# Kernel tuning notes

Hardware: AMD Instinct MI355X
Metric: run time of the kernel (lower is better)

Reference implementation:

```python
import jax, jax.numpy as jnp
import numpy as np

D_MODEL, D_QKV, N_HEADS = 1024, 64, 16


def setup_inputs() -> dict:
    key = jax.random.key(0)
    k_x, k_qkv, k_out = jax.random.split(key, 3)
    X = jax.random.normal(k_x, (2, 2048, D_MODEL), dtype=jnp.float32)
    # nn.Linear(d_model, 3*d_qkv*n_heads, bias=False): store as (in, out) for X @ W
    W_qkv = jax.random.normal(k_qkv, (D_MODEL, 3 * D_QKV * N_HEADS), dtype=jnp.float32) * (D_MODEL ** -0.5)
    W_out = jax.random.normal(k_out, (D_QKV * N_HEADS, D_MODEL), dtype=jnp.float32) * ((D_QKV * N_HEADS) ** -0.5)
    return {"X": X, "W_qkv": W_qkv, "W_out": W_out}


def reference(X, W_qkv, W_out):
    b, s, _ = X.shape
    h, d = N_HEADS, D_QKV
    scale = d ** 0.5
    qkv = X @ W_qkv                          # [b, s, 3*h*d]
    # Faithful to torch: view(b, s, h, d, 3).unbind(-1) -> interleaved q/k/v layout
    qkv = qkv.reshape(b, s, h, d, 3)
    q, k, v = qkv[..., 0], qkv[..., 1], qkv[..., 2]   # each [b, s, h, d]
    scores = jnp.einsum("bqhd,bkhd->bhqk", q, k) / scale
    weights = jax.nn.softmax(scores, axis=-1)          # [b, h, s, s]
    attn = jnp.einsum("bhqk,bkhd->bqhd", weights, v)   # [b, s, h, d]
    return attn.reshape(b, s, h * d) @ W_out           # [b, s, d_model]
```

## Files before the change

kernel.cpp:

```cpp
#include <hip/hip_runtime.h>
#include <hip/hip_bf16.h>
#include <math.h>

typedef __bf16 bf16;
typedef __bf16 bf16x4 __attribute__((ext_vector_type(4)));
typedef __bf16 bf16x8 __attribute__((ext_vector_type(8)));
typedef float f32x4 __attribute__((ext_vector_type(4)));

#define MFMA16(a, b, c) __builtin_amdgcn_mfma_f32_16x16x32_bf16(a, b, c, 0, 0, 0)

constexpr int D_MODEL = 1024;
constexpr int N_QKV   = 3072;
constexpr int BATCH   = 2;
constexpr int SEQ     = 2048;
constexpr int NH      = 16;
constexpr int DH      = 64;
constexpr int M_TOT   = BATCH * SEQ;

__device__ __forceinline__ void gl_lds16(const bf16* g, bf16* l) {
    __builtin_amdgcn_global_load_lds(
        (const __attribute__((address_space(1))) void*)g,
        (__attribute__((address_space(3))) void*)l, 16, 0, 0);
}

__device__ __forceinline__ void transpose_tile(
    const float* __restrict__ in, bf16* __restrict__ out,
    int K, int N, int n0, int k0, bf16 (*T)[72], bool permute)
{
    const int tid = threadIdx.x;
    const int r   = tid >> 2;
    const int c4  = (tid & 3) * 16;

    const float* src = in + (size_t)(k0 + r) * N + n0 + c4;
    f32x4 v0 = *(const f32x4*)(src + 0);
    f32x4 v1 = *(const f32x4*)(src + 4);
    f32x4 v2 = *(const f32x4*)(src + 8);
    f32x4 v3 = *(const f32x4*)(src + 12);
    #pragma unroll
    for (int j = 0; j < 4; j++) {
        T[c4 + j][r]      = (bf16)v0[j];
        T[c4 + 4 + j][r]  = (bf16)v1[j];
        T[c4 + 8 + j][r]  = (bf16)v2[j];
        T[c4 + 12 + j][r] = (bf16)v3[j];
    }
    __syncthreads();
    int rowg = n0 + r;
    if (permute) {
        const int which = rowg % 3;
        const int h     = rowg / 192;
        const int d     = (rowg % 192) / 3;
        rowg = which * 1024 + h * 64 + d;
    }
    bf16* dst = out + (size_t)rowg * K + k0 + c4;
    *(bf16x8*)(dst)     = *(const bf16x8*)&T[r][c4];
    *(bf16x8*)(dst + 8) = *(const bf16x8*)&T[r][c4 + 8];
}

__global__ __launch_bounds__(256) void prepass_kernel(
    const float* __restrict__ X, const float* __restrict__ Wqkv,
    const float* __restrict__ Wout,
    bf16* __restrict__ xb, bf16* __restrict__ wqkv_t, bf16* __restrict__ wout_t)
{
    __shared__ bf16 T[64][72];
    const int b = blockIdx.x;
    if (b < 2048) {
        const size_t i = ((size_t)b * 256 + threadIdx.x) * 8;
        f32x4 a0 = *(const f32x4*)(X + i);
        f32x4 a1 = *(const f32x4*)(X + i + 4);
        bf16x8 w;
        #pragma unroll
        for (int j = 0; j < 4; j++) { w[j] = (bf16)a0[j]; w[j + 4] = (bf16)a1[j]; }
        *(bf16x8*)(xb + i) = w;
    } else if (b < 2048 + 768) {
        const int idx = b - 2048;
        transpose_tile(Wqkv, wqkv_t, D_MODEL, N_QKV,
                       (idx % 48) * 64, (idx / 48) * 64, T, true);
    } else {
        const int idx = b - 2816;
        transpose_tile(Wout, wout_t, D_MODEL, D_MODEL,
                       (idx % 16) * 64, (idx / 16) * 64, T, false);
    }
}

__global__ __launch_bounds__(256) void qkv_gemm_kernel(
    const bf16* __restrict__ Xb, const bf16* __restrict__ Wt,
    bf16* __restrict__ qb, bf16* __restrict__ kb, bf16* __restrict__ vb)
{
    __shared__ __align__(16) bf16 smem[2 * 128 * 64];
    bf16* As = smem;
    bf16* Bs = smem + 128 * 64;

    const int tid  = threadIdx.x;
    const int wave = tid >> 6;
    const int lane = tid & 63;
    const int quad = lane >> 4;
    const int l16  = lane & 15;
    const int sw   = l16 & 7;
    const int m0   = blockIdx.x * 128;
    const int n0   = blockIdx.y * 128;
    const int wm   = (wave & 1) * 64;
    const int wn   = (wave >> 1) * 64;

    const int srow = lane >> 3;
    const int sc_s = ((lane & 7) ^ srow) * 8;
    const int sc_d = (lane & 7) * 8;

    f32x4 acc[4][4];
    #pragma unroll
    for (int a = 0; a < 4; a++)
        #pragma unroll
        for (int b = 0; b < 4; b++) acc[a][b] = {0.f, 0.f, 0.f, 0.f};

    for (int kb0 = 0; kb0 < D_MODEL; kb0 += 64) {
        __syncthreads();
        #pragma unroll
        for (int j = 0; j < 4; j++) {
            const int row = wave * 32 + j * 8 + srow;
            gl_lds16(Xb + (size_t)(m0 + row) * D_MODEL + kb0 + sc_s,
                     As + row * 64 + sc_d);
            gl_lds16(Wt + (size_t)(n0 + row) * D_MODEL + kb0 + sc_s,
                     Bs + row * 64 + sc_d);
        }
        __syncthreads();

        #pragma unroll
        for (int ks = 0; ks < 2; ks++) {
            const int co = ((ks * 4 + quad) ^ sw) * 8;
            bf16x8 af[4], bfr[4];
            #pragma unroll
            for (int mi = 0; mi < 4; mi++)
                af[mi] = *(const bf16x8*)&As[(wm + mi * 16 + l16) * 64 + co];
            #pragma unroll
            for (int ni = 0; ni < 4; ni++)
                bfr[ni] = *(const bf16x8*)&Bs[(wn + ni * 16 + l16) * 64 + co];
            #pragma unroll
            for (int mi = 0; mi < 4; mi++)
                #pragma unroll
                for (int ni = 0; ni < 4; ni++)
                    acc[mi][ni] = MFMA16(af[mi], bfr[ni], acc[mi][ni]);
        }
    }

    const int bb = m0 >> 11;
    if (n0 < 2048) {
        bf16* dst0 = (n0 < 1024) ? qb : kb;
        #pragma unroll
        for (int ni = 0; ni < 4; ni++) {
            const int n = n0 + wn + ni * 16 + l16;
            const int h = (n >> 6) & 15;
            const int d = n & 63;
            #pragma unroll
            for (int mi = 0; mi < 4; mi++) {
                const int s0 = (m0 + wm + mi * 16 + quad * 4) & (SEQ - 1);
                const size_t bh = (size_t)(bb * NH + h);
                #pragma unroll
                for (int i = 0; i < 4; i++)
                    dst0[(bh * SEQ + s0 + i) * DH + d] = (bf16)acc[mi][ni][i];
            }
        }
    } else {
        __syncthreads();
        bf16* T = smem;
        #pragma unroll
        for (int ni = 0; ni < 4; ni++) {
            const int nl = wn + ni * 16 + l16;
            #pragma unroll
            for (int mi = 0; mi < 4; mi++) {
                const int ml = wm + mi * 16 + quad * 4;
                bf16x4 pv;
                #pragma unroll
                for (int i = 0; i < 4; i++) pv[i] = (bf16)acc[mi][ni][i];
                const int c   = ml >> 3;
                const int swz = (c & 8) | ((c ^ nl) & 7);
                *(bf16x4*)&T[nl * 128 + swz * 8 + (ml & 7)] = pv;
            }
        }
        __syncthreads();
        const int hbase  = (n0 - 2048) >> 6;
        const int s_base = m0 & (SEQ - 1);
        #pragma unroll
        for (int it = 0; it < 8; it++) {
            const int nl = (tid >> 4) + it * 16;
            const int mc = tid & 15;
            const int swz = (mc & 8) | ((mc ^ nl) & 7);
            bf16x8 vv = *(const bf16x8*)&T[nl * 128 + swz * 8];
            const int h = hbase + (nl >> 6);
            const int d = nl & 63;
            *(bf16x8*)(vb + ((size_t)(bb * NH + h) * DH + d) * SEQ
                       + s_base + mc * 8) = vv;
        }
    }
}

__global__ __launch_bounds__(256) void attn_kernel(
    const bf16* __restrict__ qb, const bf16* __restrict__ kb,
    const bf16* __restrict__ vb, bf16* __restrict__ ob)
{
    __shared__ __align__(16) bf16 Ks[2][64 * 64];
    __shared__ __align__(16) bf16 Vt[2][64 * 64];
    __shared__ __align__(16) bf16 Ps[4][2][16][64];

    const int tid  = threadIdx.x;
    const int wave = tid >> 6;
    const int lane = tid & 63;
    const int quad = lane >> 4;
    const int l16  = lane & 15;
    const int sw   = l16 & 7;
    const int bh   = blockIdx.x;
    const int q0   = blockIdx.y * 128;
    const size_t base = (size_t)bh * SEQ * DH;

    constexpr float QSCALE = 0.125f * 1.44269504f;
    bf16x8 qf[2][2];
    #pragma unroll
    for (int qs = 0; qs < 2; qs++) {
        const size_t qoff = base + (size_t)(q0 + wave * 32 + qs * 16 + l16) * DH + quad * 8;
        qf[qs][0] = *(const bf16x8*)(qb + qoff);
        qf[qs][1] = *(const bf16x8*)(qb + qoff + 32);
        #pragma unroll
        for (int j = 0; j < 8; j++) {
            qf[qs][0][j] = (bf16)((float)qf[qs][0][j] * QSCALE);
            qf[qs][1][j] = (bf16)((float)qf[qs][1][j] * QSCALE);
        }
    }

    bf16x8 ones;
    #pragma unroll
    for (int j = 0; j < 8; j++) ones[j] = (bf16)1.0f;

    f32x4 o_acc[2][4];
    f32x4 o_l[2] = {{0.f,0.f,0.f,0.f},{0.f,0.f,0.f,0.f}};
    #pragma unroll
    for (int qs = 0; qs < 2; qs++)
        #pragma unroll
        for (int t = 0; t < 4; t++) o_acc[qs][t] = {0.f, 0.f, 0.f, 0.f};

    const int so0 = tid;
    const int so1 = 256 + tid;
    const int sr0 = so0 >> 3, sc0 = ((so0 & 7) ^ (sr0 & 7)) * 8;
    const int sr1 = so1 >> 3, sc1 = ((so1 & 7) ^ (sr1 & 7)) * 8;

    #define STAGE(bufi, kk0)                                                   \
        do {                                                                   \
            gl_lds16(kb + base + (size_t)((kk0) + sr0) * DH + sc0,             \
                     &Ks[bufi][so0 * 8]);                                      \
            gl_lds16(kb + base + (size_t)((kk0) + sr1) * DH + sc1,             \
                     &Ks[bufi][so1 * 8]);                                      \
            gl_lds16(vb + base + (size_t)sr0 * SEQ + (kk0) + sc0,              \
                     &Vt[bufi][so0 * 8]);                                      \
            gl_lds16(vb + base + (size_t)sr1 * SEQ + (kk0) + sc1,              \
                     &Vt[bufi][so1 * 8]);                                      \
        } while (0)

    STAGE(0, 0);
    int buf = 0;

    for (int k0 = 0; k0 < SEQ; k0 += 64) {
        __syncthreads();
        if (k0 + 64 < SEQ) STAGE(buf ^ 1, k0 + 64);

        f32x4 sacc[2][4];
        #pragma unroll
        for (int qs = 0; qs < 2; qs++)
            #pragma unroll
            for (int t = 0; t < 4; t++) sacc[qs][t] = {0.f, 0.f, 0.f, 0.f};
        #pragma unroll
        for (int t = 0; t < 4; t++) {
            const bf16* kr = &Ks[buf][(t * 16 + l16) * 64];
            bf16x8 kf0 = *(const bf16x8*)(kr + ((quad)     ^ sw) * 8);
            bf16x8 kf1 = *(const bf16x8*)(kr + ((4 + quad) ^ sw) * 8);
            #pragma unroll
            for (int qs = 0; qs < 2; qs++) {
                sacc[qs][t] = MFMA16(kf0, qf[qs][0], sacc[qs][t]);
                sacc[qs][t] = MFMA16(kf1, qf[qs][1], sacc[qs][t]);
            }
        }

        #pragma unroll
        for (int qs = 0; qs < 2; qs++) {
            #pragma unroll
            for (int t = 0; t < 4; t++) {
                bf16x4 pv;
                #pragma unroll
                for (int i = 0; i < 4; i++)
                    pv[i] = (bf16)__builtin_amdgcn_exp2f(sacc[qs][t][i]);
                const int c2 = (2 * t + (quad >> 1)) ^ sw;
                *(bf16x4*)&Ps[wave][qs][l16][c2 * 8 + (quad & 1) * 4] = pv;
            }
        }

        #pragma unroll
        for (int ks = 0; ks < 2; ks++) {
            const int co = ((ks * 4 + quad) ^ sw) * 8;
            bf16x8 pf0 = *(const bf16x8*)&Ps[wave][0][l16][co];
            bf16x8 pf1 = *(const bf16x8*)&Ps[wave][1][l16][co];
            o_l[0] = MFMA16(pf0, ones, o_l[0]);
            o_l[1] = MFMA16(pf1, ones, o_l[1]);
            #pragma unroll
            for (int t = 0; t < 4; t++) {
                bf16x8 vf = *(const bf16x8*)&Vt[buf][(t * 16 + l16) * 64 + co];
                o_acc[0][t] = MFMA16(pf0, vf, o_acc[0][t]);
                o_acc[1][t] = MFMA16(pf1, vf, o_acc[1][t]);
            }
        }
        buf ^= 1;
    }
    #undef STAGE

    const int b = bh >> 4, h = bh & 15;
    #pragma unroll
    for (int qs = 0; qs < 2; qs++) {
        f32x4 linv;
        #pragma unroll
        for (int i = 0; i < 4; i++) linv[i] = 1.0f / o_l[qs][i];
        #pragma unroll
        for (int t = 0; t < 4; t++) {
            #pragma unroll
            for (int i = 0; i < 4; i++) {
                const int q = q0 + wave * 32 + qs * 16 + quad * 4 + i;
                ob[((size_t)(b * SEQ + q) * NH + h) * DH + t * 16 + l16] =
                    (bf16)(o_acc[qs][t][i] * linv[i]);
            }
        }
    }
}

__global__ __launch_bounds__(256) void out_gemm_kernel(
    const bf16* __restrict__ A, const bf16* __restrict__ Wt,
    float* __restrict__ out)
{
    __shared__ __align__(16) bf16 As[128 * 64];
    __shared__ __align__(16) bf16 Bs[128 * 64];

    const int tid  = threadIdx.x;
    const int wave = tid >> 6;
    const int lane = tid & 63;
    const int quad = lane >> 4;
    const int l16  = lane & 15;
    const int sw   = l16 & 7;
    const int m0   = blockIdx.x * 128;
    const int n0   = blockIdx.y * 128;
    const int wm   = (wave & 1) * 64;
    const int wn   = (wave >> 1) * 64;

    const int srow = lane >> 3;
    const int sc_s = ((lane & 7) ^ srow) * 8;
    const int sc_d = (lane & 7) * 8;

    f32x4 acc[4][4];
    #pragma unroll
    for (int a = 0; a < 4; a++)
        #pragma unroll
        for (int b = 0; b < 4; b++) acc[a][b] = {0.f, 0.f, 0.f, 0.f};

    for (int kb0 = 0; kb0 < D_MODEL; kb0 += 64) {
        __syncthreads();
        #pragma unroll
        for (int j = 0; j < 4; j++) {
            const int row = wave * 32 + j * 8 + srow;
            gl_lds16(A  + (size_t)(m0 + row) * D_MODEL + kb0 + sc_s,
                     As + row * 64 + sc_d);
            gl_lds16(Wt + (size_t)(n0 + row) * D_MODEL + kb0 + sc_s,
                     Bs + row * 64 + sc_d);
        }
        __syncthreads();

        #pragma unroll
        for (int ks = 0; ks < 2; ks++) {
            const int co = ((ks * 4 + quad) ^ sw) * 8;
            bf16x8 af[4], bfr[4];
            #pragma unroll
            for (int mi = 0; mi < 4; mi++)
                af[mi] = *(const bf16x8*)&As[(wm + mi * 16 + l16) * 64 + co];
            #pragma unroll
            for (int ni = 0; ni < 4; ni++)
                bfr[ni] = *(const bf16x8*)&Bs[(wn + ni * 16 + l16) * 64 + co];
            #pragma unroll
            for (int mi = 0; mi < 4; mi++)
                #pragma unroll
                for (int ni = 0; ni < 4; ni++)
                    acc[mi][ni] = MFMA16(af[mi], bfr[ni], acc[mi][ni]);
        }
    }

    #pragma unroll
    for (int mi = 0; mi < 4; mi++) {
        const int row0 = m0 + wm + mi * 16 + quad * 4;
        #pragma unroll
        for (int ni = 0; ni < 4; ni++) {
            const int n = n0 + wn + ni * 16 + l16;
            #pragma unroll
            for (int i = 0; i < 4; i++)
                out[(size_t)(row0 + i) * D_MODEL + n] = acc[mi][ni][i];
        }
    }
}

extern "C" void kernel_launch(void* const* d_in, const int* in_sizes, int n_in,
                              void* d_out, int out_size, void* d_ws, size_t ws_size,
                              hipStream_t stream)
{
    const float* X    = (const float*)d_in[0];
    const float* Wqkv = (const float*)d_in[1];
    const float* Wout = (const float*)d_in[2];
    float* out        = (float*)d_out;

    const size_t n_elem = (size_t)M_TOT * D_MODEL;
    bf16* qb      = (bf16*)d_ws;
    bf16* kb      = qb + n_elem;
    bf16* vb      = kb + n_elem;
    bf16* attnb   = vb + n_elem;
    bf16* wqkv_t  = attnb + n_elem;
    bf16* wout_t  = wqkv_t + (size_t)N_QKV * D_MODEL;
    bf16* xb      = wout_t + (size_t)D_MODEL * D_MODEL;

    prepass_kernel<<<3072, 256, 0, stream>>>(X, Wqkv, Wout, xb, wqkv_t, wout_t);

    qkv_gemm_kernel<<<dim3(M_TOT / 128, N_QKV / 128), 256, 0, stream>>>(
        xb, wqkv_t, qb, kb, vb);
    attn_kernel<<<dim3(BATCH * NH, SEQ / 128), 256, 0, stream>>>(qb, kb, vb, attnb);
    out_gemm_kernel<<<dim3(M_TOT / 128, D_MODEL / 128), 256, 0, stream>>>(
        attnb, wout_t, out);
}
```

Baseline: 184.7 us.

## Switch attention to 32x32 MFMA and keep P in registers via permlane32 swap

The attention kernel moves from 16x16x32 MFMA tiles to 32x32x16 tiles for both QK^T and PV. The softmax probabilities are rearranged across lane halves with permlane32_swap instead of a round trip through shared memory, so the per-wave P buffer is removed. This is meant to cut LDS traffic and MFMA issue count, at the cost of larger accumulators and more register pressure.

```diff
diff --git a/kernel.cpp b/kernel.cpp
--- a/kernel.cpp
+++ b/kernel.cpp
@@ -3,11 +3,16 @@
 #include <math.h>
 
 typedef __bf16 bf16;
+typedef __bf16 bf16x2 __attribute__((ext_vector_type(2)));
 typedef __bf16 bf16x4 __attribute__((ext_vector_type(4)));
 typedef __bf16 bf16x8 __attribute__((ext_vector_type(8)));
 typedef float f32x4 __attribute__((ext_vector_type(4)));
+typedef float f32x16 __attribute__((ext_vector_type(16)));
+typedef int i32x2 __attribute__((ext_vector_type(2)));
+typedef int i32x4 __attribute__((ext_vector_type(4)));
 
 #define MFMA16(a, b, c) __builtin_amdgcn_mfma_f32_16x16x32_bf16(a, b, c, 0, 0, 0)
+#define MFMA32(a, b, c) __builtin_amdgcn_mfma_f32_32x32x16_bf16(a, b, c, 0, 0, 0)
 
 constexpr int D_MODEL = 1024;
 constexpr int N_QKV   = 3072;
@@ -21,6 +26,12 @@
     __builtin_amdgcn_global_load_lds(
         (const __attribute__((address_space(1))) void*)g,
         (__attribute__((address_space(3))) void*)l, 16, 0, 0);
+}
+
+__device__ __forceinline__ void pl32swap(int& a, int& b) {
+    i32x2 r = __builtin_amdgcn_permlane32_swap(a, b, false, false);
+    a = r[0];
+    b = r[1];
 }
 
 __device__ __forceinline__ void transpose_tile(
@@ -198,29 +209,27 @@
 {
     __shared__ __align__(16) bf16 Ks[2][64 * 64];
     __shared__ __align__(16) bf16 Vt[2][64 * 64];
-    __shared__ __align__(16) bf16 Ps[4][2][16][64];
 
     const int tid  = threadIdx.x;
     const int wave = tid >> 6;
     const int lane = tid & 63;
-    const int quad = lane >> 4;
-    const int l16  = lane & 15;
-    const int sw   = l16 & 7;
+    const int l32  = lane & 31;
+    const int hi   = lane >> 5;
     const int bh   = blockIdx.x;
     const int q0   = blockIdx.y * 128;
     const size_t base = (size_t)bh * SEQ * DH;
 
     constexpr float QSCALE = 0.125f * 1.44269504f;
-    bf16x8 qf[2][2];
-    #pragma unroll
-    for (int qs = 0; qs < 2; qs++) {
-        const size_t qoff = base + (size_t)(q0 + wave * 32 + qs * 16 + l16) * DH + quad * 8;
-        qf[qs][0] = *(const bf16x8*)(qb + qoff);
-        qf[qs][1] = *(const bf16x8*)(qb + qoff + 32);
-        #pragma unroll
-        for (int j = 0; j < 8; j++) {
-            qf[qs][0][j] = (bf16)((float)qf[qs][0][j] * QSCALE);
-            qf[qs][1][j] = (bf16)((float)qf[qs][1][j] * QSCALE);
+
+    bf16x8 qf[4];
+    {
+        const size_t qoff = base + (size_t)(q0 + wave * 32 + l32) * DH + hi * 8;
+        #pragma unroll
+        for (int kc = 0; kc < 4; kc++) {
+            qf[kc] = *(const bf16x8*)(qb + qoff + kc * 16);
+            #pragma unroll
+            for (int j = 0; j < 8; j++)
+                qf[kc][j] = (bf16)((float)qf[kc][j] * QSCALE);
         }
     }
 
@@ -228,12 +237,12 @@
     #pragma unroll
     for (int j = 0; j < 8; j++) ones[j] = (bf16)1.0f;
 
-    f32x4 o_acc[2][4];
-    f32x4 o_l[2] = {{0.f,0.f,0.f,0.f},{0.f,0.f,0.f,0.f}};
-    #pragma unroll
-    for (int qs = 0; qs < 2; qs++)
-        #pragma unroll
-        for (int t = 0; t < 4; t++) o_acc[qs][t] = {0.f, 0.f, 0.f, 0.f};
+    f32x16 o_acc[2];
+    f32x16 o_l;
+    #pragma unroll
+    for (int i = 0; i < 16; i++) {
+        o_acc[0][i] = 0.f; o_acc[1][i] = 0.f; o_l[i] = 0.f;
+    }
 
     const int so0 = tid;
     const int so1 = 256 + tid;
@@ -259,48 +268,50 @@
         __syncthreads();
         if (k0 + 64 < SEQ) STAGE(buf ^ 1, k0 + 64);
 
-        f32x4 sacc[2][4];
-        #pragma unroll
-        for (int qs = 0; qs < 2; qs++)
-            #pragma unroll
-            for (int t = 0; t < 4; t++) sacc[qs][t] = {0.f, 0.f, 0.f, 0.f};
-        #pragma unroll
-        for (int t = 0; t < 4; t++) {
-            const bf16* kr = &Ks[buf][(t * 16 + l16) * 64];
-            bf16x8 kf0 = *(const bf16x8*)(kr + ((quad)     ^ sw) * 8);
-            bf16x8 kf1 = *(const bf16x8*)(kr + ((4 + quad) ^ sw) * 8);
-            #pragma unroll
-            for (int qs = 0; qs < 2; qs++) {
-                sacc[qs][t] = MFMA16(kf0, qf[qs][0], sacc[qs][t]);
-                sacc[qs][t] = MFMA16(kf1, qf[qs][1], sacc[qs][t]);
-            }
-        }
-
-        #pragma unroll
-        for (int qs = 0; qs < 2; qs++) {
-            #pragma unroll
-            for (int t = 0; t < 4; t++) {
-                bf16x4 pv;
-                #pragma unroll
-                for (int i = 0; i < 4; i++)
-                    pv[i] = (bf16)__builtin_amdgcn_exp2f(sacc[qs][t][i]);
-                const int c2 = (2 * t + (quad >> 1)) ^ sw;
-                *(bf16x4*)&Ps[wave][qs][l16][c2 * 8 + (quad & 1) * 4] = pv;
-            }
-        }
-
-        #pragma unroll
-        for (int ks = 0; ks < 2; ks++) {
-            const int co = ((ks * 4 + quad) ^ sw) * 8;
-            bf16x8 pf0 = *(const bf16x8*)&Ps[wave][0][l16][co];
-            bf16x8 pf1 = *(const bf16x8*)&Ps[wave][1][l16][co];
-            o_l[0] = MFMA16(pf0, ones, o_l[0]);
-            o_l[1] = MFMA16(pf1, ones, o_l[1]);
-            #pragma unroll
-            for (int t = 0; t < 4; t++) {
-                bf16x8 vf = *(const bf16x8*)&Vt[buf][(t * 16 + l16) * 64 + co];
-                o_acc[0][t] = MFMA16(pf0, vf, o_acc[0][t]);
-                o_acc[1][t] = MFMA16(pf1, vf, o_acc[1][t]);
+        f32x16 sacc[2];
+        #pragma unroll
+        for (int i = 0; i < 16; i++) { sacc[0][i] = 0.f; sacc[1][i] = 0.f; }
+        #pragma unroll
+        for (int kc = 0; kc < 4; kc++) {
+            #pragma unroll
+            for (int kblk = 0; kblk < 2; kblk++) {
+                const int key = kblk * 32 + l32;
+                bf16x8 kf = *(const bf16x8*)
+                    &Ks[buf][key * 64 + ((2 * kc + hi) ^ (l32 & 7)) * 8];
+                sacc[kblk] = MFMA32(kf, qf[kc], sacc[kblk]);
+            }
+        }
+
+        bf16x8 pa[4];
+        #pragma unroll
+        for (int kblk = 0; kblk < 2; kblk++) {
+            int w[8];
+            #pragma unroll
+            for (int c = 0; c < 8; c++) {
+                bf16x2 t;
+                t[0] = (bf16)__builtin_amdgcn_exp2f(sacc[kblk][2 * c]);
+                t[1] = (bf16)__builtin_amdgcn_exp2f(sacc[kblk][2 * c + 1]);
+                w[c] = __builtin_bit_cast(int, t);
+            }
+            #pragma unroll
+            for (int cc = 0; cc < 2; cc++) {
+                pl32swap(w[cc * 4 + 0], w[cc * 4 + 2]);
+                pl32swap(w[cc * 4 + 1], w[cc * 4 + 3]);
+                i32x4 fi = {w[cc * 4 + 0], w[cc * 4 + 1],
+                            w[cc * 4 + 2], w[cc * 4 + 3]};
+                pa[kblk * 2 + cc] = __builtin_bit_cast(bf16x8, fi);
+            }
+        }
+
+        #pragma unroll
+        for (int kc = 0; kc < 4; kc++) {
+            o_l = MFMA32(pa[kc], ones, o_l);
+            #pragma unroll
+            for (int nb = 0; nb < 2; nb++) {
+                const int d = nb * 32 + l32;
+                bf16x8 vf = *(const bf16x8*)
+                    &Vt[buf][d * 64 + ((2 * kc + hi) ^ (l32 & 7)) * 8];
+                o_acc[nb] = MFMA32(pa[kc], vf, o_acc[nb]);
             }
         }
         buf ^= 1;
@@ -309,19 +320,13 @@
 
     const int b = bh >> 4, h = bh & 15;
     #pragma unroll
-    for (int qs = 0; qs < 2; qs++) {
-        f32x4 linv;
-        #pragma unroll
-        for (int i = 0; i < 4; i++) linv[i] = 1.0f / o_l[qs][i];
-        #pragma unroll
-        for (int t = 0; t < 4; t++) {
-            #pragma unroll
-            for (int i = 0; i < 4; i++) {
-                const int q = q0 + wave * 32 + qs * 16 + quad * 4 + i;
-                ob[((size_t)(b * SEQ + q) * NH + h) * DH + t * 16 + l16] =
-                    (bf16)(o_acc[qs][t][i] * linv[i]);
-            }
-        }
+    for (int i = 0; i < 16; i++) {
+        const int q = q0 + wave * 32 + (i & 3) + 8 * (i >> 2) + 4 * hi;
+        const float li = 1.0f / o_l[i];
+        #pragma unroll
+        for (int nb = 0; nb < 2; nb++)
+            ob[((size_t)(b * SEQ + q) * NH + h) * DH + nb * 32 + l32] =
+                (bf16)(o_acc[nb][i] * li);
     }
 }
 
```

Result: no change. 188.1 us (+1.9%).
